# Kernel optimization log

Measured on AMD Instinct MI355X. Metric: run time of the kernel, lower is better.

The kernel has to match this reference:

```python
import jax, jax.numpy as jnp
import numpy as np

NUM_BITS = 10
MEM_SIZE = 2 ** NUM_BITS  # 1024
HIDDEN = 1024
INPUT = 1024
BATCH = 16384
LN_EPS = 1e-5


def setup_inputs() -> dict:
    key = jax.random.key(0)
    ks = jax.random.split(key, 8)
    s = 0.02
    return {
        "x": jax.random.normal(ks[0], (BATCH, INPUT), jnp.float32),
        "h_prev": jax.random.normal(ks[1], (BATCH, HIDDEN), jnp.float32),
        "memory": jax.random.normal(ks[2], (MEM_SIZE, HIDDEN), jnp.float32),
        "W_w": jax.random.normal(ks[3], (HIDDEN, INPUT), jnp.float32) * s,
        "W_b": jnp.zeros((HIDDEN,), jnp.float32),
        "U_w": jax.random.normal(ks[4], (HIDDEN, HIDDEN), jnp.float32) * s,
        "U_b": jnp.zeros((HIDDEN,), jnp.float32),
        "Q_w": jax.random.normal(ks[5], (HIDDEN, HIDDEN), jnp.float32) * s,
        "Q_b": jnp.zeros((HIDDEN,), jnp.float32),
        "M_w": jax.random.normal(ks[6], (NUM_BITS, HIDDEN), jnp.float32) * s,
        "M_b": jnp.zeros((NUM_BITS,), jnp.float32),
        "ln_g": jnp.ones((HIDDEN,), jnp.float32),
        "ln_b": jnp.zeros((HIDDEN,), jnp.float32),
    }


def reference(x, h_prev, memory, W_w, W_b, U_w, U_b, Q_w, Q_b, M_w, M_b, ln_g, ln_b):
    # Binary address from h_prev (eval-mode hard threshold, non-differentiable)
    powers = jnp.asarray(2 ** np.arange(NUM_BITS - 1, -1, -1), dtype=x.dtype)  # [num_bits]
    logits = h_prev @ M_w.T + M_b                              # [B, num_bits]
    binary = (jax.nn.sigmoid(logits) > 0.5).astype(x.dtype)    # hard bits
    index = jnp.clip((binary * powers).sum(-1).astype(jnp.int32), 0, MEM_SIZE - 1)  # [B]
    h_mem = memory[index]                                      # gather [B, H]
    # Fused linear combine + LayerNorm + sigmoid
    pre = x @ W_w.T + W_b + h_prev @ U_w.T + U_b + h_mem @ Q_w.T + Q_b  # [B, H]
    mu = pre.mean(-1, keepdims=True)
    var = ((pre - mu) ** 2).mean(-1, keepdims=True)            # biased var (torch LN)
    norm = (pre - mu) * jax.lax.rsqrt(var + LN_EPS)
    return jax.nn.sigmoid(norm * ln_g + ln_b)                  # h_new [B, H]
```

## Files before the change

kernel.cpp:

```cpp
#include <hip/hip_runtime.h>

#define BATCH   16384
#define HIDDEN  1024
#define K2      2048
#define MEMSZ   1024
#define NBITS   10

#define BM 256
#define BN 256
#define BK 64
#define NT (K2 / BK)

typedef __bf16 bf16x8 __attribute__((ext_vector_type(8)));
typedef float  f32x4  __attribute__((ext_vector_type(4)));
typedef unsigned short u16x8 __attribute__((ext_vector_type(8)));

__device__ __forceinline__ unsigned short f2bf(float f) {
    unsigned int u = __float_as_uint(f);
    u += 0x7FFFu + ((u >> 16) & 1u);
    return (unsigned short)(u >> 16);
}

__device__ __forceinline__ u16x8 f2bf8(float4 a, float4 b) {
    u16x8 r;
    r[0] = f2bf(a.x); r[1] = f2bf(a.y); r[2] = f2bf(a.z); r[3] = f2bf(a.w);
    r[4] = f2bf(b.x); r[5] = f2bf(b.y); r[6] = f2bf(b.z); r[7] = f2bf(b.w);
    return r;
}

__device__ __forceinline__ void gload_lds16(const void* g, void* l) {
    __builtin_amdgcn_global_load_lds(
        (const __attribute__((address_space(1))) unsigned int*)g,
        (__attribute__((address_space(3))) unsigned int*)l,
        16, 0, 0);
}

__global__ __launch_bounds__(256) void pack_build_kernel(
        const float* __restrict__ W, const float* __restrict__ U,
        const float* __restrict__ memory, const float* __restrict__ Q,
        const float* __restrict__ x, const float* __restrict__ h_prev,
        const float* __restrict__ M_w, const float* __restrict__ M_b,
        unsigned short* __restrict__ Bm, unsigned short* __restrict__ Mem,
        unsigned short* __restrict__ Qb, unsigned short* __restrict__ A,
        int* __restrict__ idxbuf) {
    if (blockIdx.x < 2048) {
        int u = blockIdx.x * 256 + threadIdx.x;
        const float* src;
        unsigned short* dst;
        if (u < 262144) {
            int n  = u >> 8;
            int k8 = (u & 255) << 3;
            src = (k8 < 1024) ? (W + (size_t)n * 1024 + k8)
                              : (U + (size_t)n * 1024 + (k8 - 1024));
            dst = Bm + (size_t)n * K2 + k8;
        } else if (u < 393216) {
            int f = (u - 262144) << 3;
            src = memory + f;  dst = Mem + f;
        } else {
            int f = (u - 393216) << 3;
            src = Q + f;  dst = Qb + f;
        }
        float4 a = *reinterpret_cast<const float4*>(src);
        float4 b = *reinterpret_cast<const float4*>(src + 4);
        *reinterpret_cast<u16x8*>(dst) = f2bf8(a, b);
        return;
    }

    const int row  = (blockIdx.x - 2048) * 4 + (threadIdx.x >> 6);
    const int lane = threadIdx.x & 63;

    const float* hr = h_prev + (size_t)row * HIDDEN;
    const float* xr = x      + (size_t)row * HIDDEN;
    float4 hA0 = *reinterpret_cast<const float4*>(hr + lane * 8);
    float4 hA1 = *reinterpret_cast<const float4*>(hr + lane * 8 + 4);
    float4 hB0 = *reinterpret_cast<const float4*>(hr + 512 + lane * 8);
    float4 hB1 = *reinterpret_cast<const float4*>(hr + 512 + lane * 8 + 4);
    float4 xA0 = *reinterpret_cast<const float4*>(xr + lane * 8);
    float4 xA1 = *reinterpret_cast<const float4*>(xr + lane * 8 + 4);
    float4 xB0 = *reinterpret_cast<const float4*>(xr + 512 + lane * 8);
    float4 xB1 = *reinterpret_cast<const float4*>(xr + 512 + lane * 8 + 4);

    float s[NBITS];
#pragma unroll
    for (int j = 0; j < NBITS; ++j) {
        const float* mp = M_w + (size_t)j * HIDDEN;
        float4 mA0 = *reinterpret_cast<const float4*>(mp + lane * 8);
        float4 mA1 = *reinterpret_cast<const float4*>(mp + lane * 8 + 4);
        float4 mB0 = *reinterpret_cast<const float4*>(mp + 512 + lane * 8);
        float4 mB1 = *reinterpret_cast<const float4*>(mp + 512 + lane * 8 + 4);
        s[j] = (hA0.x * mA0.x + hA0.y * mA0.y + hA0.z * mA0.z + hA0.w * mA0.w)
             + (hA1.x * mA1.x + hA1.y * mA1.y + hA1.z * mA1.z + hA1.w * mA1.w)
             + (hB0.x * mB0.x + hB0.y * mB0.y + hB0.z * mB0.z + hB0.w * mB0.w)
             + (hB1.x * mB1.x + hB1.y * mB1.y + hB1.z * mB1.z + hB1.w * mB1.w);
    }
#pragma unroll
    for (int off = 32; off >= 1; off >>= 1) {
#pragma unroll
        for (int j = 0; j < NBITS; ++j) s[j] += __shfl_xor(s[j], off, 64);
    }
    int idx = 0;
#pragma unroll
    for (int j = 0; j < NBITS; ++j)
        if (s[j] + M_b[j] > 0.f) idx |= 1 << (NBITS - 1 - j);
    if (lane == 0) idxbuf[row] = idx;

    unsigned short* arow = A + (size_t)row * K2;
    *reinterpret_cast<u16x8*>(arow + lane * 8)        = f2bf8(xA0, xA1);
    *reinterpret_cast<u16x8*>(arow + 512 + lane * 8)  = f2bf8(xB0, xB1);
    *reinterpret_cast<u16x8*>(arow + 1024 + lane * 8) = f2bf8(hA0, hA1);
    *reinterpret_cast<u16x8*>(arow + 1536 + lane * 8) = f2bf8(hB0, hB1);
}

__global__ __launch_bounds__(256) void mq_kernel(
        const unsigned short* __restrict__ Mem,
        const unsigned short* __restrict__ Qb,
        float* __restrict__ MQ) {
    __shared__ unsigned short As[128 * 64];
    __shared__ unsigned short Bs[128 * 64];

    const int ks = blockIdx.x >> 6;
    const int mb = (blockIdx.x >> 3) & 7;
    const int nb = blockIdx.x & 7;
    const int t    = threadIdx.x;
    const int lane = t & 63;
    const int w    = t >> 6;
    const int wr   = w >> 1, wc = w & 1;
    const int rr   = lane & 15, rq = lane >> 4;
    const int c8   = (t & 7) * 8;
    const int srow = t >> 3;

    f32x4 acc[4][4] = {};

    for (int kt = 0; kt < 4; ++kt) {
        const int k0 = ks * 256 + kt * 64;
#pragma unroll
        for (int i = 0; i < 4; ++i) {
            int r = i * 32 + srow;
            gload_lds16(Mem + (size_t)(mb * 128 + r) * 1024 + k0 + c8, As + i * 2048 + t * 8);
            gload_lds16(Qb  + (size_t)(nb * 128 + r) * 1024 + k0 + c8, Bs + i * 2048 + t * 8);
        }
        __syncthreads();
#pragma unroll
        for (int kk = 0; kk < 2; ++kk) {
            const int krd = kk * 32 + rq * 8;
            bf16x8 af[4], bfv[4];
#pragma unroll
            for (int m = 0; m < 4; ++m)
                af[m] = *reinterpret_cast<const bf16x8*>(As + (wr * 64 + m * 16 + rr) * 64 + krd);
#pragma unroll
            for (int n = 0; n < 4; ++n)
                bfv[n] = *reinterpret_cast<const bf16x8*>(Bs + (wc * 64 + n * 16 + rr) * 64 + krd);
#pragma unroll
            for (int m = 0; m < 4; ++m)
#pragma unroll
                for (int n = 0; n < 4; ++n)
                    acc[m][n] = __builtin_amdgcn_mfma_f32_16x16x32_bf16(
                        af[m], bfv[n], acc[m][n], 0, 0, 0);
        }
        __syncthreads();
    }

#pragma unroll
    for (int m = 0; m < 4; ++m)
#pragma unroll
        for (int n = 0; n < 4; ++n) {
            int gcol = nb * 128 + wc * 64 + n * 16 + rr;
#pragma unroll
            for (int j = 0; j < 4; ++j) {
                int grow = mb * 128 + wr * 64 + m * 16 + rq * 4 + j;
                atomicAdd(&MQ[(size_t)grow * 1024 + gcol], acc[m][n][j]);
            }
        }
}


__device__ __forceinline__ void stage_g(const unsigned short* __restrict__ src,
                                        int rowbase, int kt, int g,
                                        unsigned short* ldsTile, int t) {
    const int o      = g * 8192 + t * 16;
    const int row    = o >> 7;
    const int inner  = o & 127;
    const int sinner = inner ^ ((row & 7) << 4);
    const char* gp = reinterpret_cast<const char*>(
                         src + (size_t)(rowbase + row) * K2 + kt * BK) + sinner;
    gload_lds16(gp, reinterpret_cast<char*>(ldsTile) + o);
}

__device__ __forceinline__ bf16x8 ldsfrag(const unsigned short* tile, int row,
                                          int kbyte_x_sw) {
    return *reinterpret_cast<const bf16x8*>(
        reinterpret_cast<const char*>(tile) + row * 128 + kbyte_x_sw);
}

#define PH_BAR()                                                     \
    do {                                                             \
        asm volatile("" ::: "memory");                               \
        __builtin_amdgcn_s_barrier();                                \
        asm volatile("" ::: "memory");                               \
    } while (0)

#define LGKM(N)                                                      \
    do {                                                             \
        asm volatile("s_waitcnt lgkmcnt(" #N ")" ::: "memory");      \
        __builtin_amdgcn_sched_barrier(0);                           \
    } while (0)

#define MFMA_Q(AF, BF, MB, NB)                                                 \
    {                                                                          \
        __builtin_amdgcn_s_setprio(1);                                         \
        _Pragma("unroll") for (int m_ = 0; m_ < 4; ++m_)                       \
        _Pragma("unroll") for (int n_ = 0; n_ < 2; ++n_)                       \
        _Pragma("unroll") for (int kk_ = 0; kk_ < 2; ++kk_)                    \
            acc[(MB) + m_][(NB) + n_] =                                        \
                __builtin_amdgcn_mfma_f32_16x16x32_bf16(                       \
                    AF[m_][kk_], BF[n_][kk_],                                  \
                    acc[(MB) + m_][(NB) + n_], 0, 0, 0);                       \
        __builtin_amdgcn_s_setprio(0);                                         \
    }

__global__ __launch_bounds__(512, 2) void gemm_kernel(
        const unsigned short* __restrict__ A,
        const unsigned short* __restrict__ Bm,
        float* __restrict__ C) {
    __shared__ alignas(16) unsigned short lds[2][2][BM * BK];

    const int bid  = blockIdx.x;
    const int wgid = (bid & 7) * 32 + (bid >> 3);
    const int mblk = wgid >> 2;
    const int nblk = wgid & 3;

    const int t    = threadIdx.x;
    const int lane = t & 63;
    const int w    = t >> 6;
    const int wr   = w >> 2;
    const int wc   = w & 3;
    const int rr   = lane & 15;
    const int rq   = lane >> 4;
    const int sw   = (rr & 7) << 4;
    const int rqb  = rq * 16;
    const int wrb  = wr * 128;
    const int wcb  = wc * 64;

    const int arow = mblk * BM;
    const int brow = nblk * BN;

    f32x4 acc[8][4] = {};

    {
#pragma unroll
        for (int g = 0; g < 4; ++g) stage_g(A,  arow, 0, g, &lds[0][0][0], t);
#pragma unroll
        for (int g = 0; g < 4; ++g) stage_g(Bm, brow, 0, g, &lds[0][1][0], t);
#pragma unroll
        for (int g = 0; g < 4; ++g) stage_g(Bm, brow, 1, g, &lds[1][1][0], t);
#pragma unroll
        for (int g = 0; g < 4; ++g) stage_g(A,  arow, 1, g, &lds[1][0][0], t);
        asm volatile("s_waitcnt vmcnt(8)" ::: "memory");
        asm volatile("" ::: "memory");
        __builtin_amdgcn_s_barrier();
    }

    bf16x8 af  [4][2];
    bf16x8 af2 [4][2];
    bf16x8 bfr01[2][2];
    bf16x8 bfr23[2][2];

#pragma unroll
    for (int m = 0; m < 4; ++m) {
        af[m][0] = ldsfrag(&lds[0][0][0], wrb + m * 16 + rr, (rqb) ^ sw);
        af[m][1] = ldsfrag(&lds[0][0][0], wrb + m * 16 + rr, (64 + rqb) ^ sw);
    }
#pragma unroll
    for (int n = 0; n < 2; ++n) {
        bfr01[n][0] = ldsfrag(&lds[0][1][0], wcb + n * 16 + rr, (rqb) ^ sw);
        bfr01[n][1] = ldsfrag(&lds[0][1][0], wcb + n * 16 + rr, (64 + rqb) ^ sw);
    }

    for (int kt = 0; kt < NT; ++kt) {
        const int c = kt & 1;
        const unsigned short* At  = &lds[c][0][0];
        const unsigned short* Bt  = &lds[c][1][0];
        const unsigned short* nxA = &lds[c ^ 1][0][0];
        const unsigned short* nxB = &lds[c ^ 1][1][0];
        unsigned short* curA = &lds[c][0][0];
        unsigned short* curB = &lds[c][1][0];
        const bool pf1 = (kt + 1 < NT);
        const bool pf2 = (kt + 2 < NT);

        PH_BAR();
#pragma unroll
        for (int n = 0; n < 2; ++n) {
            bfr23[n][0] = ldsfrag(Bt, wcb + 32 + n * 16 + rr, (rqb) ^ sw);
            bfr23[n][1] = ldsfrag(Bt, wcb + 32 + n * 16 + rr, (64 + rqb) ^ sw);
        }
        af2[0][0] = ldsfrag(At, wrb + 64 + rr, (rqb) ^ sw);
        af2[0][1] = ldsfrag(At, wrb + 64 + rr, (64 + rqb) ^ sw);
        LGKM(6);
        MFMA_Q(af, bfr01, 0, 0);

        PH_BAR();
#pragma unroll
        for (int m = 1; m < 4; ++m) {
            af2[m][0] = ldsfrag(At, wrb + 64 + m * 16 + rr, (rqb) ^ sw);
            af2[m][1] = ldsfrag(At, wrb + 64 + m * 16 + rr, (64 + rqb) ^ sw);
        }
        LGKM(8);
        MFMA_Q(af, bfr23, 0, 2);
        __builtin_amdgcn_sched_barrier(0);
        asm volatile("s_waitcnt vmcnt(0)" ::: "memory");
        asm volatile("" ::: "memory");

        PH_BAR();
        if (pf2) {
            stage_g(Bm, brow, kt + 2, 0, curB, t);
            stage_g(Bm, brow, kt + 2, 1, curB, t);
            stage_g(Bm, brow, kt + 2, 2, curB, t);
            stage_g(Bm, brow, kt + 2, 3, curB, t);
        }
        if (pf1) {
#pragma unroll
            for (int m = 0; m < 3; ++m) {
                af[m][0] = ldsfrag(nxA, wrb + m * 16 + rr, (rqb) ^ sw);
                af[m][1] = ldsfrag(nxA, wrb + m * 16 + rr, (64 + rqb) ^ sw);
            }
            LGKM(6);
        } else {
            LGKM(0);
        }
        MFMA_Q(af2, bfr01, 4, 0);

        PH_BAR();
        if (pf2) {
            stage_g(A, arow, kt + 2, 0, curA, t);
            stage_g(A, arow, kt + 2, 1, curA, t);
            stage_g(A, arow, kt + 2, 2, curA, t);
            stage_g(A, arow, kt + 2, 3, curA, t);
        }
        if (pf1) {
            af[3][0] = ldsfrag(nxA, wrb + 48 + rr, (rqb) ^ sw);
            af[3][1] = ldsfrag(nxA, wrb + 48 + rr, (64 + rqb) ^ sw);
#pragma unroll
            for (int n = 0; n < 2; ++n) {
                bfr01[n][0] = ldsfrag(nxB, wcb + n * 16 + rr, (rqb) ^ sw);
                bfr01[n][1] = ldsfrag(nxB, wcb + n * 16 + rr, (64 + rqb) ^ sw);
            }
        }
        MFMA_Q(af2, bfr23, 4, 2);
    }

#pragma unroll
    for (int mi = 0; mi < 8; ++mi) {
#pragma unroll
        for (int n = 0; n < 4; ++n) {
            const int gcol = nblk * BN + wcb + n * 16 + rr;
#pragma unroll
            for (int j = 0; j < 4; ++j) {
                const int grow = mblk * BM + wrb + mi * 16 + rq * 4 + j;
                C[(size_t)grow * HIDDEN + gcol] = acc[mi][n][j];
            }
        }
    }
}

__global__ __launch_bounds__(256) void ln_kernel(
        float* __restrict__ C,
        const int* __restrict__ idxbuf,
        const float* __restrict__ MQ,
        const float* __restrict__ W_b, const float* __restrict__ U_b,
        const float* __restrict__ Q_b, const float* __restrict__ ln_g,
        const float* __restrict__ ln_b) {
    const int row = blockIdx.x;
    const int t   = threadIdx.x;
    const int midx = idxbuf[row];
    float4* rowp = reinterpret_cast<float4*>(C + (size_t)row * HIDDEN);
    const float4* mqp = reinterpret_cast<const float4*>(MQ + (size_t)midx * HIDDEN);

    float4 p  = rowp[t];
    float4 mq = mqp[t];
    float4 bw = reinterpret_cast<const float4*>(W_b)[t];
    float4 bu = reinterpret_cast<const float4*>(U_b)[t];
    float4 bq = reinterpret_cast<const float4*>(Q_b)[t];
    p.x += mq.x + bw.x + bu.x + bq.x;
    p.y += mq.y + bw.y + bu.y + bq.y;
    p.z += mq.z + bw.z + bu.z + bq.z;
    p.w += mq.w + bw.w + bu.w + bq.w;

    float s  = p.x + p.y + p.z + p.w;
    float sq = p.x * p.x + p.y * p.y + p.z * p.z + p.w * p.w;
#pragma unroll
    for (int off = 32; off >= 1; off >>= 1) {
        s  += __shfl_xor(s,  off, 64);
        sq += __shfl_xor(sq, off, 64);
    }
    __shared__ float red[8];
    const int lane = t & 63, w = t >> 6;
    if (lane == 0) { red[w] = s; red[4 + w] = sq; }
    __syncthreads();
    const float S    = red[0] + red[1] + red[2] + red[3];
    const float SQ   = red[4] + red[5] + red[6] + red[7];
    const float mean = S * (1.0f / HIDDEN);
    const float var  = SQ * (1.0f / HIDDEN) - mean * mean;
    const float rstd = rsqrtf(var + 1e-5f);

    float4 g = reinterpret_cast<const float4*>(ln_g)[t];
    float4 b = reinterpret_cast<const float4*>(ln_b)[t];
    float4 o;
    o.x = 1.f / (1.f + __expf(-((p.x - mean) * rstd * g.x + b.x)));
    o.y = 1.f / (1.f + __expf(-((p.y - mean) * rstd * g.y + b.y)));
    o.z = 1.f / (1.f + __expf(-((p.z - mean) * rstd * g.z + b.z)));
    o.w = 1.f / (1.f + __expf(-((p.w - mean) * rstd * g.w + b.w)));
    rowp[t] = o;
}

extern "C" void kernel_launch(void* const* d_in, const int* in_sizes, int n_in,
                              void* d_out, int out_size, void* d_ws, size_t ws_size,
                              hipStream_t stream) {
    const float* x      = (const float*)d_in[0];
    const float* h_prev = (const float*)d_in[1];
    const float* memory = (const float*)d_in[2];
    const float* W_w    = (const float*)d_in[3];
    const float* W_b    = (const float*)d_in[4];
    const float* U_w    = (const float*)d_in[5];
    const float* U_b    = (const float*)d_in[6];
    const float* Q_w    = (const float*)d_in[7];
    const float* Q_b    = (const float*)d_in[8];
    const float* M_w    = (const float*)d_in[9];
    const float* M_b    = (const float*)d_in[10];
    const float* ln_g   = (const float*)d_in[11];
    const float* ln_b   = (const float*)d_in[12];

    char* ws = (char*)d_ws;
    unsigned short* A   = (unsigned short*)(ws);
    unsigned short* Bm  = (unsigned short*)(ws + 67108864);
    unsigned short* Mem = (unsigned short*)(ws + 71303168);
    unsigned short* Qb  = (unsigned short*)(ws + 73400320);
    float*          MQ  = (float*)         (ws + 75497472);
    int*            idx = (int*)           (ws + 79691776);
    float* pre = (float*)d_out;

    hipLaunchKernelGGL(pack_build_kernel, dim3(6144), dim3(256), 0, stream,
                       W_w, U_w, memory, Q_w, x, h_prev, M_w, M_b,
                       Bm, Mem, Qb, A, idx);
    hipMemsetAsync(MQ, 0, (size_t)MEMSZ * HIDDEN * sizeof(float), stream);
    hipLaunchKernelGGL(mq_kernel, dim3(256), dim3(256), 0, stream,
                       Mem, Qb, MQ);
    hipLaunchKernelGGL(gemm_kernel, dim3((BATCH / BM) * (HIDDEN / BN)), dim3(512), 0, stream,
                       A, Bm, pre);
    hipLaunchKernelGGL(ln_kernel, dim3(BATCH), dim3(256), 0, stream,
                       pre, idx, MQ, W_b, U_b, Q_b, ln_g, ln_b);
}
```

Measured before the change: 171.2 us.

## Split x packing into separate blocks, drop split-K atomics and memset in MQ

The x-to-bf16 conversion moves out of the per-row address blocks into extra flat conversion blocks, which leaves the address blocks lighter and holding fewer registers. The bit-logit reduction now runs one bit at a time instead of keeping ten partial sums live. The memory×Q product no longer uses split-K with atomics and a preceding memset; each block covers the full K and writes its result directly. The cost is that the MQ kernel runs on only 64 blocks with longer loops, which reduces its parallelism.

Result: no change. 173.5 us (+1.3%).

```diff
diff --git a/kernel.cpp b/kernel.cpp
--- a/kernel.cpp
+++ b/kernel.cpp
@@ -43,7 +43,7 @@
         unsigned short* __restrict__ Bm, unsigned short* __restrict__ Mem,
         unsigned short* __restrict__ Qb, unsigned short* __restrict__ A,
         int* __restrict__ idxbuf) {
-    if (blockIdx.x < 2048) {
+    if (blockIdx.x < 10240) {
         int u = blockIdx.x * 256 + threadIdx.x;
         const float* src;
         unsigned short* dst;
@@ -56,9 +56,14 @@
         } else if (u < 393216) {
             int f = (u - 262144) << 3;
             src = memory + f;  dst = Mem + f;
-        } else {
+        } else if (u < 524288) {
             int f = (u - 393216) << 3;
             src = Q + f;  dst = Qb + f;
+        } else {
+            int e = (u - 524288) << 3;
+            int row = e >> 10, col = e & 1023;
+            src = x + (size_t)row * HIDDEN + col;
+            dst = A + (size_t)row * K2 + col;
         }
         float4 a = *reinterpret_cast<const float4*>(src);
         float4 b = *reinterpret_cast<const float4*>(src + 4);
@@ -66,21 +71,16 @@
         return;
     }
 
-    const int row  = (blockIdx.x - 2048) * 4 + (threadIdx.x >> 6);
+    const int row  = (blockIdx.x - 10240) * 4 + (threadIdx.x >> 6);
     const int lane = threadIdx.x & 63;
 
     const float* hr = h_prev + (size_t)row * HIDDEN;
-    const float* xr = x      + (size_t)row * HIDDEN;
     float4 hA0 = *reinterpret_cast<const float4*>(hr + lane * 8);
     float4 hA1 = *reinterpret_cast<const float4*>(hr + lane * 8 + 4);
     float4 hB0 = *reinterpret_cast<const float4*>(hr + 512 + lane * 8);
     float4 hB1 = *reinterpret_cast<const float4*>(hr + 512 + lane * 8 + 4);
-    float4 xA0 = *reinterpret_cast<const float4*>(xr + lane * 8);
-    float4 xA1 = *reinterpret_cast<const float4*>(xr + lane * 8 + 4);
-    float4 xB0 = *reinterpret_cast<const float4*>(xr + 512 + lane * 8);
-    float4 xB1 = *reinterpret_cast<const float4*>(xr + 512 + lane * 8 + 4);
-
-    float s[NBITS];
+
+    int idx = 0;
 #pragma unroll
     for (int j = 0; j < NBITS; ++j) {
         const float* mp = M_w + (size_t)j * HIDDEN;
@@ -88,25 +88,17 @@
         float4 mA1 = *reinterpret_cast<const float4*>(mp + lane * 8 + 4);
         float4 mB0 = *reinterpret_cast<const float4*>(mp + 512 + lane * 8);
         float4 mB1 = *reinterpret_cast<const float4*>(mp + 512 + lane * 8 + 4);
-        s[j] = (hA0.x * mA0.x + hA0.y * mA0.y + hA0.z * mA0.z + hA0.w * mA0.w)
-             + (hA1.x * mA1.x + hA1.y * mA1.y + hA1.z * mA1.z + hA1.w * mA1.w)
-             + (hB0.x * mB0.x + hB0.y * mB0.y + hB0.z * mB0.z + hB0.w * mB0.w)
-             + (hB1.x * mB1.x + hB1.y * mB1.y + hB1.z * mB1.z + hB1.w * mB1.w);
-    }
-#pragma unroll
-    for (int off = 32; off >= 1; off >>= 1) {
-#pragma unroll
-        for (int j = 0; j < NBITS; ++j) s[j] += __shfl_xor(s[j], off, 64);
-    }
-    int idx = 0;
-#pragma unroll
-    for (int j = 0; j < NBITS; ++j)
-        if (s[j] + M_b[j] > 0.f) idx |= 1 << (NBITS - 1 - j);
+        float s = (hA0.x * mA0.x + hA0.y * mA0.y + hA0.z * mA0.z + hA0.w * mA0.w)
+                + (hA1.x * mA1.x + hA1.y * mA1.y + hA1.z * mA1.z + hA1.w * mA1.w)
+                + (hB0.x * mB0.x + hB0.y * mB0.y + hB0.z * mB0.z + hB0.w * mB0.w)
+                + (hB1.x * mB1.x + hB1.y * mB1.y + hB1.z * mB1.z + hB1.w * mB1.w);
+#pragma unroll
+        for (int off = 32; off >= 1; off >>= 1) s += __shfl_xor(s, off, 64);
+        if (s + M_b[j] > 0.f) idx |= 1 << (NBITS - 1 - j);
+    }
     if (lane == 0) idxbuf[row] = idx;
 
     unsigned short* arow = A + (size_t)row * K2;
-    *reinterpret_cast<u16x8*>(arow + lane * 8)        = f2bf8(xA0, xA1);
-    *reinterpret_cast<u16x8*>(arow + 512 + lane * 8)  = f2bf8(xB0, xB1);
     *reinterpret_cast<u16x8*>(arow + 1024 + lane * 8) = f2bf8(hA0, hA1);
     *reinterpret_cast<u16x8*>(arow + 1536 + lane * 8) = f2bf8(hB0, hB1);
 }
@@ -118,8 +110,7 @@
     __shared__ unsigned short As[128 * 64];
     __shared__ unsigned short Bs[128 * 64];
 
-    const int ks = blockIdx.x >> 6;
-    const int mb = (blockIdx.x >> 3) & 7;
+    const int mb = blockIdx.x >> 3;
     const int nb = blockIdx.x & 7;
     const int t    = threadIdx.x;
     const int lane = t & 63;
@@ -131,8 +122,8 @@
 
     f32x4 acc[4][4] = {};
 
-    for (int kt = 0; kt < 4; ++kt) {
-        const int k0 = ks * 256 + kt * 64;
+    for (int kt = 0; kt < 16; ++kt) {
+        const int k0 = kt * 64;
 #pragma unroll
         for (int i = 0; i < 4; ++i) {
             int r = i * 32 + srow;
@@ -168,7 +159,7 @@
 #pragma unroll
             for (int j = 0; j < 4; ++j) {
                 int grow = mb * 128 + wr * 64 + m * 16 + rq * 4 + j;
-                atomicAdd(&MQ[(size_t)grow * 1024 + gcol], acc[m][n][j]);
+                MQ[(size_t)grow * 1024 + gcol] = acc[m][n][j];
             }
         }
 }
@@ -438,11 +429,10 @@
     int*            idx = (int*)           (ws + 79691776);
     float* pre = (float*)d_out;
 
-    hipLaunchKernelGGL(pack_build_kernel, dim3(6144), dim3(256), 0, stream,
+    hipLaunchKernelGGL(pack_build_kernel, dim3(14336), dim3(256), 0, stream,
                        W_w, U_w, memory, Q_w, x, h_prev, M_w, M_b,
                        Bm, Mem, Qb, A, idx);
-    hipMemsetAsync(MQ, 0, (size_t)MEMSZ * HIDDEN * sizeof(float), stream);
-    hipLaunchKernelGGL(mq_kernel, dim3(256), dim3(256), 0, stream,
+    hipLaunchKernelGGL(mq_kernel, dim3(64), dim3(256), 0, stream,
                        Mem, Qb, MQ);
     hipLaunchKernelGGL(gemm_kernel, dim3((BATCH / BM) * (HIDDEN / BN)), dim3(512), 0, stream,
                        A, Bm, pre);
```
